# Performance work log

Measured on AMD Instinct MI355X. Metric: run time of the kernel, lower is better.

Reference implementation:

```python
import jax, jax.numpy as jnp
import numpy as np

N_NODES = 50000
N_EDGES = 800000
IN_DIM = 256
OUT_DIM = 768
D_SCALE = OUT_DIM // 3  # 256, must equal IN_DIM so repeated conv application type-checks
SCALES = [1, 2, 4]


def setup_inputs() -> dict:
    key = jax.random.key(0)
    ks = jax.random.split(key, 12)
    x = jax.random.normal(ks[0], (N_NODES, IN_DIM), dtype=jnp.float32)
    edge_index = jax.random.randint(ks[1], (2, N_EDGES), 0, N_NODES, dtype=jnp.int64)
    edge_attr = jax.random.uniform(ks[2], (N_EDGES, 1), dtype=jnp.float32)
    s = 1.0 / np.sqrt(IN_DIM)
    W1 = jax.random.uniform(ks[3], (IN_DIM, D_SCALE), jnp.float32, -s, s)
    b1 = jnp.zeros((D_SCALE,), jnp.float32)
    W2 = jax.random.uniform(ks[4], (IN_DIM, D_SCALE), jnp.float32, -s, s)
    b2 = jnp.zeros((D_SCALE,), jnp.float32)
    W3 = jax.random.uniform(ks[5], (IN_DIM, D_SCALE), jnp.float32, -s, s)
    b3 = jnp.zeros((D_SCALE,), jnp.float32)
    sp = 1.0 / np.sqrt(OUT_DIM)
    Wp = jax.random.uniform(ks[6], (OUT_DIM, OUT_DIM), jnp.float32, -sp, sp)
    bp = jax.random.uniform(ks[7], (OUT_DIM,), jnp.float32, -sp, sp)
    gamma = jnp.ones((OUT_DIM,), jnp.float32)
    beta = jnp.zeros((OUT_DIM,), jnp.float32)
    return {"x": x, "edge_index": edge_index, "edge_attr": edge_attr,
            "W1": W1, "b1": b1, "W2": W2, "b2": b2, "W3": W3, "b3": b3,
            "Wp": Wp, "bp": bp, "gamma": gamma, "beta": beta}


def _gcn_conv(x, src, dst, norm, W, b):
    # PyG GCNConv: h = x @ W; out[i] = sum_{(j->i)} norm_e * h[j]; + bias
    h = x @ W                                   # [N, D]
    msg = h[src] * norm[:, None]                # [E+N, D] edge gather (memory-bound)
    out = jax.ops.segment_sum(msg, dst, num_segments=N_NODES)
    return out + b


def reference(x, edge_index, edge_attr, W1, b1, W2, b2, W3, b3, Wp, bp, gamma, beta):
    ew = edge_attr.squeeze(-1)
    src = edge_index[0]
    dst = edge_index[1]
    # add self-loops with weight 1 (GCNConv default, fill_value=1)
    loop = jnp.arange(N_NODES, dtype=src.dtype)
    src_a = jnp.concatenate([src, loop])
    dst_a = jnp.concatenate([dst, loop])
    w_a = jnp.concatenate([ew, jnp.ones((N_NODES,), ew.dtype)])
    deg = jax.ops.segment_sum(w_a, dst_a, num_segments=N_NODES)
    dinv = jnp.where(deg > 0, jax.lax.rsqrt(deg), 0.0)
    norm = dinv[src_a] * w_a * dinv[dst_a]      # symmetric normalization per edge

    feats = []
    for (W, b), scale in zip([(W1, b1), (W2, b2), (W3, b3)], SCALES):
        f = x
        for _ in range(scale):
            f = _gcn_conv(f, src_a, dst_a, norm, W, b)
        feats.append(f)
    out = jnp.concatenate(feats, axis=1)        # [N, OUT_DIM]
    out = out @ Wp + bp
    mu = jnp.mean(out, axis=-1, keepdims=True)
    var = jnp.var(out, axis=-1, keepdims=True)
    out = (out - mu) * jax.lax.rsqrt(var + 1e-5) * gamma + beta
    return jax.nn.gelu(out, approximate=False)
```

## Files before the change

kernel.cpp:

```cpp
#include <hip/hip_runtime.h>
#include <math.h>

#define NN 50000
#define NE 800000
#define DIN 256
#define DOUT 768
#define NPAD 50176

typedef _Float16 half8 __attribute__((ext_vector_type(8)));
typedef _Float16 half4 __attribute__((ext_vector_type(4)));
typedef float    f32x4 __attribute__((ext_vector_type(4)));

__global__ void init_deg_cnt(float* __restrict__ deg, int* __restrict__ cnt) {
    int i = blockIdx.x * 256 + threadIdx.x;
    if (i < NN) { deg[i] = 1.0f; cnt[i] = 0; }
}

__global__ void edge_deg_cnt(const int* __restrict__ ei, const float* __restrict__ ea,
                             float* __restrict__ deg, int* __restrict__ cnt) {
    int e = blockIdx.x * 256 + threadIdx.x;
    if (e >= NE) return;
    int dst = ei[NE + e];
    atomicAdd(&deg[dst], ea[e]);
    atomicAdd(&cnt[dst], 1);
}

__global__ void compute_dinv(const float* __restrict__ deg, float* __restrict__ dinv) {
    int i = blockIdx.x * 256 + threadIdx.x;
    if (i < NN) { float d = deg[i]; dinv[i] = d > 0.f ? rsqrtf(d) : 0.f; }
}

__global__ __launch_bounds__(1024) void scan_kernel(
        const int* __restrict__ cnt, int* __restrict__ row_ptr,
        int* __restrict__ cursor) {
    __shared__ int ssum[1024];
    int t = threadIdx.x;
    const int chunk = (NN + 1023) / 1024;
    int beg = t * chunk;
    int end = beg + chunk; if (end > NN) end = NN;
    int s = 0;
    for (int i = beg; i < end; ++i) s += cnt[i];
    ssum[t] = s;
    __syncthreads();
    if (t == 0) {
        int run = 0;
        for (int i = 0; i < 1024; ++i) { int v = ssum[i]; ssum[i] = run; run += v; }
    }
    __syncthreads();
    int run = ssum[t];
    for (int i = beg; i < end; ++i) {
        row_ptr[i] = run; cursor[i] = run; run += cnt[i];
    }
    if (t == 0) row_ptr[NN] = NE;
}

__global__ void edge_scatter(const int* __restrict__ ei, const float* __restrict__ ea,
                             const float* __restrict__ dinv, int* __restrict__ cursor,
                             int* __restrict__ col, float* __restrict__ val) {
    int e = blockIdx.x * 256 + threadIdx.x;
    if (e >= NE) return;
    int s = ei[e];
    int d = ei[NE + e];
    int pos = atomicAdd(&cursor[d], 1);
    col[pos] = s;
    val[pos] = dinv[s] * ea[e] * dinv[d];
}

__global__ void x2h_kernel(const float* __restrict__ x, _Float16* __restrict__ Xh) {
    int i = blockIdx.x * 256 + threadIdx.x;
    if (i >= NN * DIN / 4) return;
    float4 v = ((const float4*)x)[i];
    half4 h; h[0] = (_Float16)v.x; h[1] = (_Float16)v.y;
    h[2] = (_Float16)v.z; h[3] = (_Float16)v.w;
    ((half4*)Xh)[i] = h;
}

__device__ inline float rv(const float* __restrict__ R, int c) {
    return R ? R[c] : 1.f;
}

__global__ __launch_bounds__(256) void agg_kernel(
        const _Float16* __restrict__ Gin, int sIn,
        _Float16* __restrict__ Gout, int sOut,
        const float* __restrict__ Rin, float* __restrict__ Rout,
        const int* __restrict__ rowp, const int* __restrict__ colv,
        const float* __restrict__ val, const float* __restrict__ dinv) {
    int node = blockIdx.x * 4 + (threadIdx.x >> 6);
    if (node >= NN) return;
    int lane = threadIdx.x & 63;
    const _Float16* gb = Gin + lane * 4;
    float acc[4] = {0.f, 0.f, 0.f, 0.f};
    float racc = 0.f;
    int beg = rowp[node], end = rowp[node + 1];
    int k = beg;
    for (; k + 8 <= end; k += 8) {
        int   c0 = colv[k+0], c1 = colv[k+1], c2 = colv[k+2], c3 = colv[k+3];
        int   c4 = colv[k+4], c5 = colv[k+5], c6 = colv[k+6], c7 = colv[k+7];
        float v0 = val[k+0], v1 = val[k+1], v2 = val[k+2], v3 = val[k+3];
        float v4 = val[k+4], v5 = val[k+5], v6 = val[k+6], v7 = val[k+7];
        half4 g0 = *(const half4*)(gb + (size_t)c0 * sIn);
        half4 g1 = *(const half4*)(gb + (size_t)c1 * sIn);
        half4 g2 = *(const half4*)(gb + (size_t)c2 * sIn);
        half4 g3 = *(const half4*)(gb + (size_t)c3 * sIn);
        half4 g4 = *(const half4*)(gb + (size_t)c4 * sIn);
        half4 g5 = *(const half4*)(gb + (size_t)c5 * sIn);
        half4 g6 = *(const half4*)(gb + (size_t)c6 * sIn);
        half4 g7 = *(const half4*)(gb + (size_t)c7 * sIn);
#pragma unroll
        for (int j = 0; j < 4; ++j)
            acc[j] += v0 * (float)g0[j] + v1 * (float)g1[j]
                    + v2 * (float)g2[j] + v3 * (float)g3[j]
                    + v4 * (float)g4[j] + v5 * (float)g5[j]
                    + v6 * (float)g6[j] + v7 * (float)g7[j];
        if (Rout)
            racc += v0 * rv(Rin, c0) + v1 * rv(Rin, c1)
                  + v2 * rv(Rin, c2) + v3 * rv(Rin, c3)
                  + v4 * rv(Rin, c4) + v5 * rv(Rin, c5)
                  + v6 * rv(Rin, c6) + v7 * rv(Rin, c7);
    }
    for (; k + 4 <= end; k += 4) {
        int   c0 = colv[k+0], c1 = colv[k+1], c2 = colv[k+2], c3 = colv[k+3];
        float v0 = val[k+0], v1 = val[k+1], v2 = val[k+2], v3 = val[k+3];
        half4 g0 = *(const half4*)(gb + (size_t)c0 * sIn);
        half4 g1 = *(const half4*)(gb + (size_t)c1 * sIn);
        half4 g2 = *(const half4*)(gb + (size_t)c2 * sIn);
        half4 g3 = *(const half4*)(gb + (size_t)c3 * sIn);
#pragma unroll
        for (int j = 0; j < 4; ++j)
            acc[j] += v0 * (float)g0[j] + v1 * (float)g1[j]
                    + v2 * (float)g2[j] + v3 * (float)g3[j];
        if (Rout)
            racc += v0 * rv(Rin, c0) + v1 * rv(Rin, c1)
                  + v2 * rv(Rin, c2) + v3 * rv(Rin, c3);
    }
    for (; k < end; ++k) {
        int c = colv[k]; float v = val[k];
        half4 g = *(const half4*)(gb + (size_t)c * sIn);
#pragma unroll
        for (int j = 0; j < 4; ++j) acc[j] += v * (float)g[j];
        if (Rout) racc += v * rv(Rin, c);
    }
    float dv = dinv[node], sv = dv * dv;
    half4 gs = *(const half4*)(gb + (size_t)node * sIn);
#pragma unroll
    for (int j = 0; j < 4; ++j) acc[j] += sv * (float)gs[j];
    half4 o;
#pragma unroll
    for (int j = 0; j < 4; ++j) o[j] = (_Float16)acc[j];
    *(half4*)(Gout + (size_t)node * sOut + lane * 4) = o;
    if (Rout && lane == 0)
        Rout[node] = racc + sv * (Rin ? Rin[node] : 1.f);
}

__global__ __launch_bounds__(256) void wp1(
        const float* __restrict__ W2, const float* __restrict__ W3,
        const float* __restrict__ b2, const float* __restrict__ b3,
        float* __restrict__ W2sq, float* __restrict__ W3_2,
        float* __restrict__ bw2, float* __restrict__ bw3a) {
    int b = blockIdx.x, j = threadIdx.x;
    const float* A; const float* B; float* C;
    if (b < 256)      { A = W2 + b * 256;         B = W2; C = W2sq + b * 256; }
    else if (b < 512) { A = W3 + (b - 256) * 256; B = W3; C = W3_2 + (b - 256) * 256; }
    else if (b == 512){ A = b2;                   B = W2; C = bw2; }
    else              { A = b3;                   B = W3; C = bw3a; }
    float s = 0.f;
#pragma unroll 8
    for (int k = 0; k < 256; ++k) s += A[k] * B[k * 256 + j];
    C[j] = s;
}

__global__ __launch_bounds__(256) void wp2(
        const float* __restrict__ W3_2, const float* __restrict__ W3,
        const float* __restrict__ bw3a,
        float* __restrict__ W3_4, float* __restrict__ bw3b) {
    int b = blockIdx.x, j = threadIdx.x;
    const float* A; const float* B; float* C;
    if (b < 256) { A = W3_2 + b * 256; B = W3_2; C = W3_4 + b * 256; }
    else         { A = bw3a;           B = W3;   C = bw3b; }
    float s = 0.f;
#pragma unroll 8
    for (int k = 0; k < 256; ++k) s += A[k] * B[k * 256 + j];
    C[j] = s;
}

__global__ __launch_bounds__(256) void wp3(
        const float* __restrict__ W1, const float* __restrict__ W2sq,
        const float* __restrict__ W3_4, const float* __restrict__ Wp,
        const float* __restrict__ W3, const float* __restrict__ bw3b,
        _Float16* __restrict__ Mt, float* __restrict__ bw3c) {
    int b = blockIdx.x, j = threadIdx.x;
    if (b == 768) {
        float s = 0.f;
#pragma unroll 8
        for (int k = 0; k < 256; ++k) s += bw3b[k] * W3[k * 256 + j];
        bw3c[j] = s;
        return;
    }
    int kk = b;
    int blk = kk >> 8;
    const float* A = (blk == 0) ? (W1 + kk * 256)
                   : (blk == 1) ? (W2sq + (kk - 256) * 256)
                                : (W3_4 + (kk - 512) * 256);
    const float* B = Wp + (size_t)(blk * 256) * 768;
    float s0 = 0.f, s1 = 0.f, s2 = 0.f;
#pragma unroll 4
    for (int m = 0; m < 256; ++m) {
        float a = A[m];
        const float* br = B + (size_t)m * 768;
        s0 += a * br[j]; s1 += a * br[j + 256]; s2 += a * br[j + 512];
    }
    Mt[(size_t)j * 768 + kk]         = (_Float16)s0;
    Mt[(size_t)(j + 256) * 768 + kk] = (_Float16)s1;
    Mt[(size_t)(j + 512) * 768 + kk] = (_Float16)s2;
}

__global__ __launch_bounds__(256) void wp4(
        const float* __restrict__ Wp,
        const float* __restrict__ b1, const float* __restrict__ b2,
        const float* __restrict__ b3, const float* __restrict__ bp,
        const float* __restrict__ bw2, const float* __restrict__ bw3a,
        const float* __restrict__ bw3b, const float* __restrict__ bw3c,
        float* __restrict__ u1, float* __restrict__ u2,
        float* __restrict__ u3, float* __restrict__ c0) {
    int vec = blockIdx.x / 3, chunk = blockIdx.x % 3;
    int j = chunk * 256 + threadIdx.x;
    const float* P1 = Wp;
    const float* P2 = Wp + (size_t)256 * 768;
    const float* P3 = Wp + (size_t)512 * 768;
    float s = 0.f;
    if (vec == 0) {
#pragma unroll 8
        for (int k = 0; k < 256; ++k) s += bw2[k] * P2[(size_t)k * 768 + j];
#pragma unroll 8
        for (int k = 0; k < 256; ++k) s += bw3a[k] * P3[(size_t)k * 768 + j];
        u1[j] = s;
    } else if (vec == 1) {
#pragma unroll 8
        for (int k = 0; k < 256; ++k) s += bw3b[k] * P3[(size_t)k * 768 + j];
        u2[j] = s;
    } else if (vec == 2) {
#pragma unroll 8
        for (int k = 0; k < 256; ++k) s += bw3c[k] * P3[(size_t)k * 768 + j];
        u3[j] = s;
    } else {
#pragma unroll 8
        for (int k = 0; k < 256; ++k) s += b1[k] * P1[(size_t)k * 768 + j];
#pragma unroll 8
        for (int k = 0; k < 256; ++k) s += b2[k] * P2[(size_t)k * 768 + j];
#pragma unroll 8
        for (int k = 0; k < 256; ++k) s += b3[k] * P3[(size_t)k * 768 + j];
        c0[j] = s + bp[j];
    }
}

__device__ inline void g2lds16(const void* g, void* l) {
    __builtin_amdgcn_global_load_lds(
        (__attribute__((address_space(1))) void*)g,
        (__attribute__((address_space(3))) void*)l, 16, 0, 0);
}

__global__ __launch_bounds__(256) void gemm_mfma(
        const _Float16* __restrict__ A,
        const _Float16* __restrict__ Bt,
        float* __restrict__ C, int M,
        const float* __restrict__ R1, const float* __restrict__ R2,
        const float* __restrict__ R3,
        const float* __restrict__ u1, const float* __restrict__ u2,
        const float* __restrict__ u3, const float* __restrict__ c0) {
    __shared__ _Float16 As[2][128 * 32];
    __shared__ _Float16 Bs[2][128 * 32];
    const int tid  = threadIdx.x;
    const int wid  = tid >> 6;
    const int lane = tid & 63;
    const int lid  = blockIdx.y * (DOUT / 128) + blockIdx.x;
    const int pair = (lid & 7) * (NPAD / 128 * (DOUT / 128) / 8) + (lid >> 3);
    const int bm = (pair / (DOUT / 128)) * 128;
    const int bn = (pair % (DOUT / 128)) * 128;
    const int wm = (wid >> 1) * 64;
    const int wn = (wid & 1) * 64;
    const int l15  = lane & 15;
    const int quad = lane >> 4;

    f32x4 acc[4][4] = {};

    const int srow_in_grp = lane >> 2;
    const int schunk      = lane & 3;

    auto stage = [&](int buf, int k0) {
#pragma unroll
        for (int q = 0; q < 2; ++q) {
            int row = wid * 32 + q * 16 + srow_in_grp;
            int gchunk = (schunk - ((row >> 1) & 3)) & 3;
            const _Float16* ga = A  + (size_t)(bm + row) * DOUT + k0 + gchunk * 8;
            const _Float16* gb = Bt + (size_t)(bn + row) * DOUT + k0 + gchunk * 8;
            g2lds16(ga, &As[buf][(size_t)(wid * 32 + q * 16) * 32]);
            g2lds16(gb, &Bs[buf][(size_t)(wid * 32 + q * 16) * 32]);
        }
    };

    const int NT = DOUT / 32;
    stage(0, 0);
    __syncthreads();
    int cur = 0;
    for (int t = 0; t < NT; ++t) {
        if (t + 1 < NT) stage(cur ^ 1, (t + 1) * 32);
        half8 af[4], bfr[4];
#pragma unroll
        for (int i = 0; i < 4; ++i) {
            int ra = wm + i * 16 + l15;
            int pa = (quad + ((ra >> 1) & 3)) & 3;
            af[i] = *(const half8*)(&As[cur][(size_t)ra * 32 + pa * 8]);
            int rb = wn + i * 16 + l15;
            int pb = (quad + ((rb >> 1) & 3)) & 3;
            bfr[i] = *(const half8*)(&Bs[cur][(size_t)rb * 32 + pb * 8]);
        }
#pragma unroll
        for (int mi = 0; mi < 4; ++mi)
#pragma unroll
            for (int ni = 0; ni < 4; ++ni)
                acc[mi][ni] = __builtin_amdgcn_mfma_f32_16x16x32_f16(
                    af[mi], bfr[ni], acc[mi][ni], 0, 0, 0);
        __syncthreads();
        cur ^= 1;
    }

    float e0[4], e1[4], e2[4], e3[4];
#pragma unroll
    for (int ni = 0; ni < 4; ++ni) {
        int gc = bn + wn + ni * 16 + l15;
        e0[ni] = c0[gc]; e1[ni] = u1[gc]; e2[ni] = u2[gc]; e3[ni] = u3[gc];
    }
#pragma unroll
    for (int mi = 0; mi < 4; ++mi) {
#pragma unroll
        for (int r = 0; r < 4; ++r) {
            int gr = bm + wm + mi * 16 + quad * 4 + r;
            if (gr >= M) continue;
            float r1 = R1[gr], r2 = R2[gr], r3 = R3[gr];
#pragma unroll
            for (int ni = 0; ni < 4; ++ni) {
                int gc = bn + wn + ni * 16 + l15;
                C[(size_t)gr * DOUT + gc] =
                    acc[mi][ni][r] + e0[ni] + r1 * e1[ni] + r2 * e2[ni] + r3 * e3[ni];
            }
        }
    }
}

__global__ __launch_bounds__(256) void ln_gelu_kernel(float* __restrict__ out,
        const float* __restrict__ gamma, const float* __restrict__ beta) {
    int row = blockIdx.x;
    int t = threadIdx.x;
    float* p = out + (size_t)row * DOUT;
    float x0 = p[t], x1 = p[t + 256], x2 = p[t + 512];
    float s = x0 + x1 + x2;
    float s2 = x0 * x0 + x1 * x1 + x2 * x2;
    __shared__ float red[8];
    int wave = t >> 6, lane = t & 63;
#pragma unroll
    for (int m = 1; m < 64; m <<= 1) {
        s += __shfl_xor(s, m);
        s2 += __shfl_xor(s2, m);
    }
    if (lane == 0) { red[wave] = s; red[4 + wave] = s2; }
    __syncthreads();
    float S = red[0] + red[1] + red[2] + red[3];
    float S2 = red[4] + red[5] + red[6] + red[7];
    float mu = S * (1.f / 768.f);
    float var = S2 * (1.f / 768.f) - mu * mu;
    float inv = rsqrtf(var + 1e-5f);
    const float kk = 0.70710678118654752f;
#pragma unroll
    for (int i = 0; i < 3; ++i) {
        int c = t + 256 * i;
        float x = (i == 0) ? x0 : (i == 1) ? x1 : x2;
        float y = (x - mu) * inv * gamma[c] + beta[c];
        p[c] = 0.5f * y * (1.f + erff(y * kk));
    }
}

extern "C" void kernel_launch(void* const* d_in, const int* in_sizes, int n_in,
                              void* d_out, int out_size, void* d_ws, size_t ws_size,
                              hipStream_t stream) {
    const float* x     = (const float*)d_in[0];
    const int*   ei    = (const int*)d_in[1];
    const float* ea    = (const float*)d_in[2];
    const float* W1    = (const float*)d_in[3];
    const float* b1    = (const float*)d_in[4];
    const float* W2    = (const float*)d_in[5];
    const float* b2    = (const float*)d_in[6];
    const float* W3    = (const float*)d_in[7];
    const float* b3    = (const float*)d_in[8];
    const float* Wp    = (const float*)d_in[9];
    const float* bp    = (const float*)d_in[10];
    const float* gamma = (const float*)d_in[11];
    const float* beta  = (const float*)d_in[12];
    float* out = (float*)d_out;

    char* w = (char*)d_ws;
    auto alloc = [&](size_t bytes) -> void* {
        void* p = (void*)w;
        w += (bytes + 255) & ~(size_t)255;
        return p;
    };
    _Float16* Acat = (_Float16*)alloc((size_t)NPAD * DOUT * 2);
    _Float16* Xh   = (_Float16*)alloc((size_t)NN * DIN * 2);
    _Float16* G3h  = (_Float16*)alloc((size_t)NN * DIN * 2);
    _Float16* Mt   = (_Float16*)alloc((size_t)DOUT * DOUT * 2);
    int*   col    = (int*)alloc((size_t)NE * 4);
    float* val    = (float*)alloc((size_t)NE * 4);
    float* deg    = (float*)alloc((size_t)NN * 4);
    float* dinv   = (float*)alloc((size_t)NN * 4);
    int*   cnt    = (int*)alloc((size_t)NN * 4);
    int*   rowp   = (int*)alloc((size_t)(NN + 1) * 4);
    int*   cursor = (int*)alloc((size_t)NN * 4);
    float* R1     = (float*)alloc((size_t)NN * 4);
    float* R2     = (float*)alloc((size_t)NN * 4);
    float* R3     = (float*)alloc((size_t)NN * 4);
    float* W2sq   = (float*)alloc(256 * 256 * 4);
    float* W3_2   = (float*)alloc(256 * 256 * 4);
    float* W3_4   = (float*)alloc(256 * 256 * 4);
    float* bw2    = (float*)alloc(256 * 4);
    float* bw3a   = (float*)alloc(256 * 4);
    float* bw3b   = (float*)alloc(256 * 4);
    float* bw3c   = (float*)alloc(256 * 4);
    float* u1     = (float*)alloc(768 * 4);
    float* u2     = (float*)alloc(768 * 4);
    float* u3     = (float*)alloc(768 * 4);
    float* c0     = (float*)alloc(768 * 4);

    const int nb_n = (NN + 255) / 256;
    const int nb_e = (NE + 255) / 256;

    init_deg_cnt<<<nb_n, 256, 0, stream>>>(deg, cnt);
    edge_deg_cnt<<<nb_e, 256, 0, stream>>>(ei, ea, deg, cnt);
    compute_dinv<<<nb_n, 256, 0, stream>>>(deg, dinv);
    scan_kernel<<<1, 1024, 0, stream>>>(cnt, rowp, cursor);
    edge_scatter<<<nb_e, 256, 0, stream>>>(ei, ea, dinv, cursor, col, val);

    x2h_kernel<<<(NN * DIN / 4 + 255) / 256, 256, 0, stream>>>(x, Xh);

    wp1<<<514, 256, 0, stream>>>(W2, W3, b2, b3, W2sq, W3_2, bw2, bw3a);
    wp2<<<257, 256, 0, stream>>>(W3_2, W3, bw3a, W3_4, bw3b);
    wp3<<<769, 256, 0, stream>>>(W1, W2sq, W3_4, Wp, W3, bw3b, Mt, bw3c);
    wp4<<<12, 256, 0, stream>>>(Wp, b1, b2, b3, bp, bw2, bw3a, bw3b, bw3c,
                                u1, u2, u3, c0);

    const int nb_a = (NN + 3) / 4;
    agg_kernel<<<nb_a, 256, 0, stream>>>(Xh, DIN,          Acat + 0,   DOUT, nullptr, R1, rowp, col, val, dinv);
    agg_kernel<<<nb_a, 256, 0, stream>>>(Acat + 0,   DOUT, Acat + 256, DOUT, R1,      R2, rowp, col, val, dinv);
    agg_kernel<<<nb_a, 256, 0, stream>>>(Acat + 256, DOUT, G3h,        DIN,  R2,      R3, rowp, col, val, dinv);
    agg_kernel<<<nb_a, 256, 0, stream>>>(G3h,        DIN,  Acat + 512, DOUT, nullptr, nullptr, rowp, col, val, dinv);

    dim3 grid(DOUT / 128, NPAD / 128);
    gemm_mfma<<<grid, 256, 0, stream>>>(Acat, Mt, out, NN, R1, R2, R3, u1, u2, u3, c0);

    ln_gelu_kernel<<<NN, 256, 0, stream>>>(out, gamma, beta);
}
```

Measured before the change: 973.6 us.

## Parallelize CSR prefix scan across blocks and deepen GEMM K-tile to 64

Replaces the single-block 1024-thread serial-chunk scan with a three-kernel multi-block scan (block sums, block offsets, write) built on wave shuffles, so the row-pointer build no longer runs serially on one CU. Separately, the MFMA GEMM now stages 64-wide K tiles instead of 32, with a new 8-chunk XOR-style LDS swizzle, which halves the number of barrier iterations at the cost of twice the LDS per block. Adds two extra kernel launches and may lower GEMM occupancy because of the larger shared-memory footprint.

```diff
diff --git a/kernel.cpp b/kernel.cpp
--- a/kernel.cpp
+++ b/kernel.cpp
@@ -6,6 +6,7 @@
 #define DIN 256
 #define DOUT 768
 #define NPAD 50176
+#define NBS 196
 
 typedef _Float16 half8 __attribute__((ext_vector_type(8)));
 typedef _Float16 half4 __attribute__((ext_vector_type(4)));
@@ -30,28 +31,60 @@
     if (i < NN) { float d = deg[i]; dinv[i] = d > 0.f ? rsqrtf(d) : 0.f; }
 }
 
-__global__ __launch_bounds__(1024) void scan_kernel(
-        const int* __restrict__ cnt, int* __restrict__ row_ptr,
-        int* __restrict__ cursor) {
-    __shared__ int ssum[1024];
+__global__ __launch_bounds__(256) void scan_bsum(const int* __restrict__ cnt,
+                                                 int* __restrict__ bsum) {
+    int i = blockIdx.x * 256 + threadIdx.x;
+    int v = (i < NN) ? cnt[i] : 0;
+#pragma unroll
+    for (int m = 1; m < 64; m <<= 1) v += __shfl_xor(v, m);
+    __shared__ int ws[4];
+    int wave = threadIdx.x >> 6, lane = threadIdx.x & 63;
+    if (lane == 0) ws[wave] = v;
+    __syncthreads();
+    if (threadIdx.x == 0) bsum[blockIdx.x] = ws[0] + ws[1] + ws[2] + ws[3];
+}
+
+__global__ __launch_bounds__(256) void scan_boff(const int* __restrict__ bsum,
+                                                 int* __restrict__ boff) {
     int t = threadIdx.x;
-    const int chunk = (NN + 1023) / 1024;
-    int beg = t * chunk;
-    int end = beg + chunk; if (end > NN) end = NN;
-    int s = 0;
-    for (int i = beg; i < end; ++i) s += cnt[i];
-    ssum[t] = s;
+    int v = (t < NBS) ? bsum[t] : 0;
+    int lane = t & 63, wave = t >> 6, orig = v;
+#pragma unroll
+    for (int d = 1; d < 64; d <<= 1) {
+        int u = __shfl_up(v, d);
+        if (lane >= d) v += u;
+    }
+    __shared__ int ws[4];
+    if (lane == 63) ws[wave] = v;
     __syncthreads();
-    if (t == 0) {
-        int run = 0;
-        for (int i = 0; i < 1024; ++i) { int v = ssum[i]; ssum[i] = run; run += v; }
-    }
+    int wp = 0;
+#pragma unroll
+    for (int w2 = 0; w2 < 4; ++w2) if (w2 < wave) wp += ws[w2];
+    if (t < NBS) boff[t] = wp + v - orig;
+}
+
+__global__ __launch_bounds__(256) void scan_write(const int* __restrict__ cnt,
+                                                  const int* __restrict__ boff,
+                                                  int* __restrict__ rowp,
+                                                  int* __restrict__ cursor) {
+    int b = blockIdx.x, t = threadIdx.x;
+    int i = b * 256 + t;
+    int v = (i < NN) ? cnt[i] : 0;
+    int lane = t & 63, wave = t >> 6, orig = v;
+#pragma unroll
+    for (int d = 1; d < 64; d <<= 1) {
+        int u = __shfl_up(v, d);
+        if (lane >= d) v += u;
+    }
+    __shared__ int ws[4];
+    if (lane == 63) ws[wave] = v;
     __syncthreads();
-    int run = ssum[t];
-    for (int i = beg; i < end; ++i) {
-        row_ptr[i] = run; cursor[i] = run; run += cnt[i];
-    }
-    if (t == 0) row_ptr[NN] = NE;
+    int wp = 0;
+#pragma unroll
+    for (int w2 = 0; w2 < 4; ++w2) if (w2 < wave) wp += ws[w2];
+    int excl = boff[b] + wp + v - orig;
+    if (i < NN) { rowp[i] = excl; cursor[i] = excl; }
+    if (i == NN - 1) rowp[NN] = NE;
 }
 
 __global__ void edge_scatter(const int* __restrict__ ei, const float* __restrict__ ea,
@@ -267,8 +300,8 @@
         const float* __restrict__ R3,
         const float* __restrict__ u1, const float* __restrict__ u2,
         const float* __restrict__ u3, const float* __restrict__ c0) {
-    __shared__ _Float16 As[2][128 * 32];
-    __shared__ _Float16 Bs[2][128 * 32];
+    __shared__ _Float16 As[2][128 * 64];
+    __shared__ _Float16 Bs[2][128 * 64];
     const int tid  = threadIdx.x;
     const int wid  = tid >> 6;
     const int lane = tid & 63;
@@ -283,43 +316,46 @@
 
     f32x4 acc[4][4] = {};
 
-    const int srow_in_grp = lane >> 2;
-    const int schunk      = lane & 3;
-
     auto stage = [&](int buf, int k0) {
 #pragma unroll
-        for (int q = 0; q < 2; ++q) {
-            int row = wid * 32 + q * 16 + srow_in_grp;
-            int gchunk = (schunk - ((row >> 1) & 3)) & 3;
-            const _Float16* ga = A  + (size_t)(bm + row) * DOUT + k0 + gchunk * 8;
-            const _Float16* gb = Bt + (size_t)(bn + row) * DOUT + k0 + gchunk * 8;
-            g2lds16(ga, &As[buf][(size_t)(wid * 32 + q * 16) * 32]);
-            g2lds16(gb, &Bs[buf][(size_t)(wid * 32 + q * 16) * 32]);
+        for (int it = 0; it < 4; ++it) {
+            int row = wid * 32 + it * 8 + (lane >> 3);
+            int lc  = ((lane & 7) - row) & 7;
+            const _Float16* ga = A  + (size_t)(bm + row) * DOUT + k0 + lc * 8;
+            const _Float16* gb = Bt + (size_t)(bn + row) * DOUT + k0 + lc * 8;
+            g2lds16(ga, &As[buf][(size_t)(wid * 32 + it * 8) * 64]);
+            g2lds16(gb, &Bs[buf][(size_t)(wid * 32 + it * 8) * 64]);
         }
     };
 
-    const int NT = DOUT / 32;
+    const int NT = DOUT / 64;
     stage(0, 0);
     __syncthreads();
     int cur = 0;
     for (int t = 0; t < NT; ++t) {
-        if (t + 1 < NT) stage(cur ^ 1, (t + 1) * 32);
-        half8 af[4], bfr[4];
+        if (t + 1 < NT) stage(cur ^ 1, (t + 1) * 64);
+        half8 af[2][4], bf[2][4];
 #pragma unroll
         for (int i = 0; i < 4; ++i) {
             int ra = wm + i * 16 + l15;
-            int pa = (quad + ((ra >> 1) & 3)) & 3;
-            af[i] = *(const half8*)(&As[cur][(size_t)ra * 32 + pa * 8]);
             int rb = wn + i * 16 + l15;
-            int pb = (quad + ((rb >> 1) & 3)) & 3;
-            bfr[i] = *(const half8*)(&Bs[cur][(size_t)rb * 32 + pb * 8]);
+#pragma unroll
+            for (int h = 0; h < 2; ++h) {
+                int pa = ((h * 4 + quad) + ra) & 7;
+                af[h][i] = *(const half8*)(&As[cur][(size_t)ra * 64 + pa * 8]);
+                int pb = ((h * 4 + quad) + rb) & 7;
+                bf[h][i] = *(const half8*)(&Bs[cur][(size_t)rb * 64 + pb * 8]);
+            }
         }
 #pragma unroll
         for (int mi = 0; mi < 4; ++mi)
 #pragma unroll
-            for (int ni = 0; ni < 4; ++ni)
+            for (int ni = 0; ni < 4; ++ni) {
                 acc[mi][ni] = __builtin_amdgcn_mfma_f32_16x16x32_f16(
-                    af[mi], bfr[ni], acc[mi][ni], 0, 0, 0);
+                    af[0][mi], bf[0][ni], acc[mi][ni], 0, 0, 0);
+                acc[mi][ni] = __builtin_amdgcn_mfma_f32_16x16x32_f16(
+                    af[1][mi], bf[1][ni], acc[mi][ni], 0, 0, 0);
+            }
         __syncthreads();
         cur ^= 1;
     }
@@ -414,6 +450,8 @@
     int*   cnt    = (int*)alloc((size_t)NN * 4);
     int*   rowp   = (int*)alloc((size_t)(NN + 1) * 4);
     int*   cursor = (int*)alloc((size_t)NN * 4);
+    int*   bsum   = (int*)alloc((size_t)NBS * 4);
+    int*   boff   = (int*)alloc((size_t)NBS * 4);
     float* R1     = (float*)alloc((size_t)NN * 4);
     float* R2     = (float*)alloc((size_t)NN * 4);
     float* R3     = (float*)alloc((size_t)NN * 4);
@@ -435,7 +473,9 @@
     init_deg_cnt<<<nb_n, 256, 0, stream>>>(deg, cnt);
     edge_deg_cnt<<<nb_e, 256, 0, stream>>>(ei, ea, deg, cnt);
     compute_dinv<<<nb_n, 256, 0, stream>>>(deg, dinv);
-    scan_kernel<<<1, 1024, 0, stream>>>(cnt, rowp, cursor);
+    scan_bsum<<<NBS, 256, 0, stream>>>(cnt, bsum);
+    scan_boff<<<1, 256, 0, stream>>>(bsum, boff);
+    scan_write<<<NBS, 256, 0, stream>>>(cnt, boff, rowp, cursor);
     edge_scatter<<<nb_e, 256, 0, stream>>>(ei, ea, dinv, cursor, col, val);
 
     x2h_kernel<<<(NN * DIN / 4 + 255) / 256, 256, 0, stream>>>(x, Xh);
```

New measurement: 860.8 us. 11.6% less time.
